# Optimization experiments

Hardware: AMD Instinct MI355X
Metric: run time of the kernel (lower is better)

Reference implementation:

```python
import jax, jax.numpy as jnp
from jax import lax
import numpy as np

CONF_THRES = 0.55
IOU_THRES = 0.45
MAX_DET = 1000
MAX_WH = 7680.0   # class offset for class-aware NMS (agnostic=False)
K = 4096          # NMS candidate cap (yolov5 max_nms analogue, jit-static)
IMG = 640         # letterboxed network input size
B, N, NC = 16, 25200, 80


def setup_inputs() -> dict:
    key = jax.random.key(0)
    k1, k2, k3, k4 = jax.random.split(key, 4)
    cxcy = jax.random.uniform(k1, (B, N, 2), jnp.float32, 0.0, IMG)
    wh = jax.random.uniform(k2, (B, N, 2), jnp.float32, 2.0, 120.0)
    obj = jax.random.uniform(k3, (B, N, 1), jnp.float32) ** 4
    cls = jax.random.uniform(k4, (B, N, NC), jnp.float32)
    pred = jnp.concatenate([cxcy, wh, obj, cls], axis=-1)  # [B, N, 5+NC]
    return {"pred": pred, "img0_h": 1080, "img0_w": 1920}


def xywh2xyxy(x):
    cx, cy, w, h = x[..., 0], x[..., 1], x[..., 2], x[..., 3]
    return jnp.stack([cx - w / 2, cy - h / 2, cx + w / 2, cy + h / 2], axis=-1)


def box_iou(a, b):
    # a: [K,4], b: [K,4] xyxy -> [K,K]
    lt = jnp.maximum(a[:, None, :2], b[None, :, :2])
    rb = jnp.minimum(a[:, None, 2:], b[None, :, 2:])
    wh = jnp.clip(rb - lt, 0.0)
    inter = wh[..., 0] * wh[..., 1]
    area_a = (a[:, 2] - a[:, 0]) * (a[:, 3] - a[:, 1])
    area_b = (b[:, 2] - b[:, 0]) * (b[:, 3] - b[:, 1])
    return inter / (area_a[:, None] + area_b[None, :] - inter + 1e-7)


def _nms_image(p, img0_h, img0_w):
    # p: [N, 5+NC]
    obj = p[:, 4]
    cls_conf = p[:, 5:] * obj[:, None]          # conf = obj * cls
    conf = cls_conf.max(axis=-1)
    cls_id = cls_conf.argmax(axis=-1)
    valid = (obj > CONF_THRES) & (conf > CONF_THRES)
    score = jnp.where(valid, conf, -1.0)
    # top-K candidates, sorted by confidence (descending)
    top_scores, top_idx = lax.top_k(score, K)
    boxes = xywh2xyxy(p[top_idx, :4])           # [K,4]
    cl = cls_id[top_idx].astype(p.dtype)        # [K]
    iou = box_iou(boxes + cl[:, None] * MAX_WH, boxes + cl[:, None] * MAX_WH)
    idx = jnp.arange(K)
    keep0 = top_scores > 0.0

    def body(i, keep):
        # suppress i if a higher-scoring kept box overlaps it too much
        sup = jnp.any(keep & (idx < i) & (iou[:, i] > IOU_THRES))
        return keep.at[i].set(keep[i] & ~sup)

    keep = lax.fori_loop(0, K, body, keep0)
    kept_score = jnp.where(keep, top_scores, -1.0)
    fs, fi = lax.top_k(kept_score, MAX_DET)
    fb = boxes[fi]                              # [MAX_DET,4]
    fc = cl[fi]
    fvalid = fs > 0.0
    # scale_boxes: letterboxed 640x640 -> original img0
    gain = min(IMG / img0_h, IMG / img0_w)
    pad_x = (IMG - img0_w * gain) / 2
    pad_y = (IMG - img0_h * gain) / 2
    fb = (fb - jnp.array([pad_x, pad_y, pad_x, pad_y], fb.dtype)) / gain
    fb = jnp.clip(fb, 0.0, jnp.array([img0_w, img0_h, img0_w, img0_h], fb.dtype))
    fb = jnp.round(fb)
    det = jnp.concatenate([fb, fs[:, None], fc[:, None]], axis=-1)  # [MAX_DET,6]
    return jnp.where(fvalid[:, None], det, 0.0)


def reference(pred, img0_h, img0_w):
    return jax.vmap(lambda p: _nms_image(p, img0_h, img0_w))(pred)
```

## Files before the change

### kernel.cpp

```cpp
#include <hip/hip_runtime.h>

#define BB 16
#define NN 25200
#define NC 80
#define ROWL 85
#define KTOP 4096
#define MAXDET 1000
#define CONF_T 0.55f
#define IOU_T 0.45f
#define MAX_WH_F 7680.0f
#define CNT_STRIDE 32
#define PCNT_STRIDE 16
#define CCAP 256
#define NBIN 2048

#define OFF_CNT   81920
#define OFF_KCNT  83968
#define OFF_BUCK  86016
#define OFF_KEPT  2707456
#define ZERO_WORDS 21504

__global__ void zero_kernel(unsigned int* __restrict__ w) {
  w[blockIdx.x * 256 + threadIdx.x] = 0u;
}

__global__ __launch_bounds__(256) void score_kernel(const float* __restrict__ pred,
                             unsigned long long* __restrict__ buckets,
                             unsigned int* __restrict__ pcnt,
                             unsigned int* __restrict__ cnt) {
  const int b = blockIdx.y;
  const int lane = threadIdx.x & 63;
  const int a0 = blockIdx.x * 256 + (threadIdx.x & ~63);
  const int a = a0 + lane;
  const int g = lane >> 4;
  const int gl = lane & 15;
  const float* __restrict__ pb = pred + (size_t)b * NN * ROWL;
  float obj = 0.0f;
  if (a < NN) obj = pb[(size_t)a * ROWL + 4];
  unsigned long long mask = __ballot(obj > CONF_T);
  unsigned int nvacc = 0;
  while (mask) {
    int s0 = __ffsll(mask) - 1; mask &= mask - 1;
    int s1 = -1, s2 = -1, s3 = -1;
    if (mask) { s1 = __ffsll(mask) - 1; mask &= mask - 1; }
    if (mask) { s2 = __ffsll(mask) - 1; mask &= mask - 1; }
    if (mask) { s3 = __ffsll(mask) - 1; mask &= mask - 1; }
    const int sg = (g == 0) ? s0 : (g == 1) ? s1 : (g == 2) ? s2 : s3;
    const bool act = (sg >= 0);
    const int srow = act ? sg : s0;
    const int aa = a0 + srow;
    const float objg = __shfl(obj, srow, 64);
    const float* __restrict__ row = pb + (size_t)aa * ROWL;
    float best = -1.0f; int bi = gl;
    #pragma unroll
    for (int t = 0; t < 5; ++t) {
      float v = row[5 + gl + 16 * t] * objg;
      if (v > best) { best = v; bi = gl + 16 * t; }
    }
    #pragma unroll
    for (int off = 1; off <= 8; off <<= 1) {
      float ov = __shfl_xor(best, off, 64);
      int oi = __shfl_xor(bi, off, 64);
      if (ov > best || (ov == best && oi < bi)) { best = ov; bi = oi; }
    }
    bool emit = act && (gl == 0) && (best > CONF_T);
    if (emit) {
      unsigned long long key =
          ((unsigned long long)__float_as_uint(best) << 32) |
          ((unsigned long long)((~(unsigned)aa) & 0xFFFFu) << 16) |
          (unsigned long long)(unsigned)bi;
      unsigned int slot = atomicAdd(&pcnt[(b * NC + bi) * PCNT_STRIDE], 1u);
      if (slot < CCAP)
        buckets[((size_t)(b * NC + bi) << 8) + slot] = key;
    }
    unsigned long long em = __ballot(emit);
    if (lane == 0) nvacc += (unsigned int)__popcll(em);
  }
  if (lane == 0 && nvacc)
    atomicAdd(&cnt[b * CNT_STRIDE], nvacc);
}

__device__ __forceinline__ bool iou_sup(float ax1, float ay1, float ax2, float ay2,
                                        float aar, float bx1, float by1, float bx2,
                                        float by2, float bar) {
  float ltx = fmaxf(ax1, bx1), lty = fmaxf(ay1, by1);
  float rbx = fminf(ax2, bx2), rby = fminf(ay2, by2);
  float wv = rbx - ltx; wv = wv > 0.0f ? wv : 0.0f;
  float hv = rby - lty; hv = hv > 0.0f ? hv : 0.0f;
  float inter = wv * hv;
  float iou = inter / (aar + bar - inter + 1e-7f);
  return iou > IOU_T;
}

__global__ __launch_bounds__(64) void class_nms_kernel(
    const float* __restrict__ pred,
    const unsigned long long* __restrict__ buckets,
    const unsigned int* __restrict__ pcnt,
    const unsigned int* __restrict__ cnt,
    unsigned long long* __restrict__ kept,
    unsigned int* __restrict__ kcnt) {
  const int c = blockIdx.x;
  const int b = blockIdx.y;
  const int lane = threadIdx.x;
  unsigned int pc = pcnt[(b * NC + c) * PCNT_STRIDE];
  int n_c = (int)(pc < (unsigned)CCAP ? pc : (unsigned)CCAP);
  const unsigned long long* __restrict__ bk = buckets + ((size_t)(b * NC + c) << 8);
  const float* __restrict__ pb = pred + (size_t)b * NN * ROWL;
  const float offc = (float)c * MAX_WH_F;
  const int count = (int)cnt[b * CNT_STRIDE];

  if (n_c == 0) return;

  if (n_c <= 64 && count <= KTOP) {
    unsigned long long v0 = (lane < n_c) ? bk[lane] : 0ull;
    for (int k2 = 2; k2 <= 64; k2 <<= 1) {
      for (int j = k2 >> 1; j >= 1; j >>= 1) {
        unsigned long long vo = __shfl_xor(v0, j, 64);
        bool desc = ((lane & k2) == 0);
        bool low = ((lane & j) == 0);
        if ((desc == low) ? (vo > v0) : (vo < v0)) v0 = vo;
      }
    }
    float x1 = 0.f, y1 = 0.f, x2 = 0.f, y2 = 0.f, aar = 0.f;
    const bool inr = (lane < n_c);
    if (inr) {
      unsigned int lo = (unsigned int)v0;
      int aa = (int)((~(lo >> 16)) & 0xFFFFu);
      const float* row = pb + (size_t)aa * ROWL;
      float cx = row[0], cy = row[1], w2 = row[2], h2 = row[3];
      x1 = (cx - w2 / 2.0f) + offc;
      y1 = (cy - h2 / 2.0f) + offc;
      x2 = (cx + w2 / 2.0f) + offc;
      y2 = (cy + h2 / 2.0f) + offc;
      aar = (x2 - x1) * (y2 - y1);
    }
    unsigned long long rowreg = 0ull;
    for (int i2 = 0; i2 < n_c; ++i2) {
      float bx1 = __shfl(x1, i2, 64), by1 = __shfl(y1, i2, 64);
      float bx2 = __shfl(x2, i2, 64), by2 = __shfl(y2, i2, 64);
      float bar = __shfl(aar, i2, 64);
      bool sup = inr && (lane > i2) &&
                 iou_sup(bx1, by1, bx2, by2, bar, x1, y1, x2, y2, aar);
      unsigned long long rm = __ballot(sup);
      if (lane == i2) rowreg = rm;
    }
    unsigned long long cand = (n_c >= 64) ? ~0ull : ((1ull << n_c) - 1ull);
    unsigned long long keepm = 0ull;
    while (cand) {
      int i = __ffsll(cand) - 1;
      keepm |= (1ull << i);
      unsigned long long rowi = __shfl(rowreg, i, 64);
      cand &= ~rowi;
      cand &= ~(1ull << i);
    }
    int keep0 = (int)((keepm >> lane) & 1ull);
    unsigned long long m0 = __ballot(keep0 != 0);
    int tot = (int)__popcll(m0);
    unsigned int base3 = 0;
    if (lane == 0) base3 = atomicAdd(&kcnt[b * CNT_STRIDE], (unsigned int)tot);
    base3 = (unsigned int)__shfl((int)base3, 0, 64);
    if (keep0) {
      unsigned int slot = base3 + (unsigned int)__popcll(m0 & ((1ull << lane) - 1ull));
      if (slot < (unsigned)KTOP) kept[(size_t)b * KTOP + slot] = v0;
    }
    return;
  }

  unsigned long long v[4];
  #pragma unroll
  for (int r = 0; r < 4; ++r) {
    int e = (r << 6) + lane;
    v[r] = (e < n_c) ? bk[e] : 0ull;
  }
  if (count > KTOP) {
    unsigned long long T = 0ull;
    for (int bit = 63; bit >= 0; --bit) {
      unsigned long long T2 = T | (1ull << bit);
      int cge = 0;
      for (int c2 = 0; c2 < NC; ++c2) {
        unsigned int p2 = pcnt[(b * NC + c2) * PCNT_STRIDE];
        int n2 = (int)(p2 < (unsigned)CCAP ? p2 : (unsigned)CCAP);
        const unsigned long long* bk2 = buckets + ((size_t)(b * NC + c2) << 8);
        for (int base2 = 0; base2 < n2; base2 += 64) {
          int i = base2 + lane;
          bool ge = (i < n2) && (bk2[i] >= T2);
          cge += (int)__popcll(__ballot(ge));
        }
      }
      if (cge >= KTOP) T = T2;
    }
    #pragma unroll
    for (int r = 0; r < 4; ++r) if (v[r] < T) v[r] = 0ull;
    n_c = 0;
    #pragma unroll
    for (int r = 0; r < 4; ++r) n_c += (int)__popcll(__ballot(v[r] != 0ull));
    if (n_c == 0) return;
  }
  for (int k2 = 2; k2 <= 256; k2 <<= 1) {
    if (k2 == 256) {
      #pragma unroll
      for (int r = 0; r < 2; ++r) {
        unsigned e = (unsigned)((r << 6) + lane);
        bool desc = ((e & k2) == 0);
        unsigned long long lo_ = v[r], hi_ = v[r + 2];
        bool sw = desc ? (lo_ < hi_) : (lo_ > hi_);
        v[r] = sw ? hi_ : lo_; v[r + 2] = sw ? lo_ : hi_;
      }
    }
    if (k2 >= 128) {
      #pragma unroll
      for (int rr = 0; rr < 2; ++rr) {
        int r = rr * 2;
        unsigned e = (unsigned)((r << 6) + lane);
        bool desc = ((e & k2) == 0);
        unsigned long long lo_ = v[r], hi_ = v[r + 1];
        bool sw = desc ? (lo_ < hi_) : (lo_ > hi_);
        v[r] = sw ? hi_ : lo_; v[r + 1] = sw ? lo_ : hi_;
      }
    }
    int j0 = (k2 >> 1) < 32 ? (k2 >> 1) : 32;
    for (int j = j0; j >= 1; j >>= 1) {
      #pragma unroll
      for (int r = 0; r < 4; ++r) {
        unsigned e = (unsigned)((r << 6) + lane);
        unsigned long long vo = __shfl_xor(v[r], j, 64);
        bool desc = ((e & k2) == 0);
        bool low = ((e & j) == 0);
        if ((desc == low) ? (vo > v[r]) : (vo < v[r])) v[r] = vo;
      }
    }
  }
  float x1r[4], y1r[4], x2r[4], y2r[4], ar[4];
  int keepr[4];
  #pragma unroll
  for (int r = 0; r < 4; ++r) {
    int e = (r << 6) + lane;
    keepr[r] = 0; x1r[r] = 0.f; y1r[r] = 0.f; x2r[r] = 0.f; y2r[r] = 0.f; ar[r] = 0.f;
    if (e < n_c) {
      unsigned int lo = (unsigned int)v[r];
      int aa = (int)((~(lo >> 16)) & 0xFFFFu);
      const float* row = pb + (size_t)aa * ROWL;
      float cx = row[0], cy = row[1], w2 = row[2], h2 = row[3];
      x1r[r] = (cx - w2 / 2.0f) + offc;
      y1r[r] = (cy - h2 / 2.0f) + offc;
      x2r[r] = (cx + w2 / 2.0f) + offc;
      y2r[r] = (cy + h2 / 2.0f) + offc;
      ar[r] = (x2r[r] - x1r[r]) * (y2r[r] - y1r[r]);
      keepr[r] = 1;
    }
  }
  for (int i2 = 0; i2 < n_c; ++i2) {
    int ci = i2 >> 6, li = i2 & 63;
    int ki; float bx1v, by1v, bx2v, by2v, bav;
    #define BCAST(R) { ki = __shfl(keepr[R], li, 64); bx1v = __shfl(x1r[R], li, 64); \
                       by1v = __shfl(y1r[R], li, 64); bx2v = __shfl(x2r[R], li, 64); \
                       by2v = __shfl(y2r[R], li, 64); bav = __shfl(ar[R], li, 64); }
    switch (ci) {
      case 0: BCAST(0); break;
      case 1: BCAST(1); break;
      case 2: BCAST(2); break;
      default: BCAST(3); break;
    }
    #undef BCAST
    if (!ki) continue;
    #pragma unroll
    for (int r = 0; r < 4; ++r) {
      int e = (r << 6) + lane;
      if (keepr[r] && e > i2 &&
          iou_sup(bx1v, by1v, bx2v, by2v, bav, x1r[r], y1r[r], x2r[r], y2r[r], ar[r]))
        keepr[r] = 0;
    }
  }
  unsigned long long m[4];
  int tot = 0;
  #pragma unroll
  for (int r = 0; r < 4; ++r) {
    m[r] = __ballot(keepr[r] != 0);
    tot += (int)__popcll(m[r]);
  }
  unsigned int base3 = 0;
  if (lane == 0) base3 = atomicAdd(&kcnt[b * CNT_STRIDE], (unsigned int)tot);
  base3 = (unsigned int)__shfl((int)base3, 0, 64);
  unsigned int start = base3;
  #pragma unroll
  for (int r = 0; r < 4; ++r) {
    if (keepr[r]) {
      unsigned int slot = start + (unsigned int)__popcll(m[r] & ((1ull << lane) - 1ull));
      if (slot < (unsigned)KTOP) kept[(size_t)b * KTOP + slot] = v[r];
    }
    start += (unsigned int)__popcll(m[r]);
  }
}

__global__ __launch_bounds__(1024) void finalize_kernel(
    const float* __restrict__ pred,
    const unsigned long long* __restrict__ kept,
    const unsigned int* __restrict__ kcnt,
    const int* __restrict__ ihp, const int* __restrict__ iwp,
    float* __restrict__ out) {
  __shared__ unsigned int hist[NBIN];
  __shared__ unsigned int sufx[NBIN];
  __shared__ unsigned int curs[NBIN];
  __shared__ unsigned int scanbuf[1024];
  __shared__ unsigned long long skey[KTOP];
  const int b = blockIdx.x;
  const int tid = threadIdx.x;
  unsigned int kcr = kcnt[b * CNT_STRIDE];
  const int kc = (int)(kcr < (unsigned)KTOP ? kcr : (unsigned)KTOP);
  const unsigned long long* __restrict__ kb = kept + (size_t)b * KTOP;

  for (int i = tid; i < NBIN; i += 1024) hist[i] = 0u;
  __syncthreads();

  unsigned long long myk[4];
  int myb[4];
  #pragma unroll
  for (int r = 0; r < 4; ++r) {
    int i = tid + (r << 10);
    myb[r] = -1; myk[r] = 0ull;
    if (i < kc) {
      unsigned long long k = kb[i];
      int bin = (int)((k >> 44) & (unsigned long long)(NBIN - 1));
      myk[r] = k; myb[r] = bin;
      atomicAdd(&hist[bin], 1u);
    }
  }
  __syncthreads();

  unsigned int h0 = hist[2 * tid], h1 = hist[2 * tid + 1];
  unsigned int val = h0 + h1;
  scanbuf[tid] = val;
  __syncthreads();
  for (int off = 1; off < 1024; off <<= 1) {
    unsigned int add = (tid + off < 1024) ? scanbuf[tid + off] : 0u;
    __syncthreads();
    val += add;
    scanbuf[tid] = val;
    __syncthreads();
  }
  unsigned int excl = val - (h0 + h1);
  sufx[2 * tid] = excl + h1;
  sufx[2 * tid + 1] = excl;
  curs[2 * tid] = excl + h1;
  curs[2 * tid + 1] = excl;
  __syncthreads();

  #pragma unroll
  for (int r = 0; r < 4; ++r) {
    if (myb[r] >= 0) {
      unsigned int p = atomicAdd(&curs[myb[r]], 1u);
      skey[p] = myk[r];
    }
  }
  __syncthreads();

  const int h = ihp[0], w3 = iwp[0];
  const double gd = fmin(640.0 / (double)h, 640.0 / (double)w3);
  const float gain = (float)gd;
  const float padx = (float)((640.0 - (double)w3 * gd) * 0.5);
  const float pady = (float)((640.0 - (double)h * gd) * 0.5);
  const float wf = (float)w3, hf = (float)h;
  #pragma unroll
  for (int r = 0; r < 4; ++r) {
    if (myb[r] >= 0) {
      unsigned long long k = myk[r];
      unsigned int gstart = sufx[myb[r]];
      unsigned int gcnt = hist[myb[r]];
      unsigned int rank = gstart;
      for (unsigned int j = 0; j < gcnt; ++j)
        rank += (skey[gstart + j] > k) ? 1u : 0u;
      if (rank < MAXDET) {
        unsigned int lo = (unsigned int)k;
        int aa = (int)((~(lo >> 16)) & 0xFFFFu);
        int cls = (int)(lo & 0xFFFFu);
        float score = __uint_as_float((unsigned int)(k >> 32));
        const float* row = pred + ((size_t)b * NN + aa) * ROWL;
        float cx = row[0], cy = row[1], wd = row[2], ht = row[3];
        float x1 = cx - wd / 2.0f, y1 = cy - ht / 2.0f;
        float x2 = cx + wd / 2.0f, y2 = cy + ht / 2.0f;
        x1 = rintf(fminf(fmaxf((x1 - padx) / gain, 0.0f), wf));
        y1 = rintf(fminf(fmaxf((y1 - pady) / gain, 0.0f), hf));
        x2 = rintf(fminf(fmaxf((x2 - padx) / gain, 0.0f), wf));
        y2 = rintf(fminf(fmaxf((y2 - pady) / gain, 0.0f), hf));
        float* o = out + ((size_t)b * MAXDET + (int)rank) * 6;
        o[0] = x1; o[1] = y1; o[2] = x2; o[3] = y2;
        o[4] = score; o[5] = (float)cls;
      }
    }
  }
  for (int i = kc + tid; i < MAXDET; i += 1024) {
    float* o = out + ((size_t)b * MAXDET + i) * 6;
    o[0] = 0.0f; o[1] = 0.0f; o[2] = 0.0f; o[3] = 0.0f; o[4] = 0.0f; o[5] = 0.0f;
  }
}

extern "C" void kernel_launch(void* const* d_in, const int* in_sizes, int n_in,
                              void* d_out, int out_size, void* d_ws, size_t ws_size,
                              hipStream_t stream) {
  const float* pred = (const float*)d_in[0];
  const int* ih = (const int*)d_in[1];
  const int* iw = (const int*)d_in[2];
  float* out = (float*)d_out;
  char* ws = (char*)d_ws;

  unsigned int* pcnt = (unsigned int*)ws;
  unsigned int* cnt = (unsigned int*)(ws + OFF_CNT);
  unsigned int* kcnt = (unsigned int*)(ws + OFF_KCNT);
  unsigned long long* buckets = (unsigned long long*)(ws + OFF_BUCK);
  unsigned long long* kept = (unsigned long long*)(ws + OFF_KEPT);

  zero_kernel<<<ZERO_WORDS / 256, 256, 0, stream>>>((unsigned int*)ws);
  dim3 sgrid((NN + 255) / 256, BB);
  score_kernel<<<sgrid, 256, 0, stream>>>(pred, buckets, pcnt, cnt);
  dim3 cgrid(NC, BB);
  class_nms_kernel<<<cgrid, 64, 0, stream>>>(pred, buckets, pcnt, cnt, kept, kcnt);
  finalize_kernel<<<BB, 1024, 0, stream>>>(pred, kept, kcnt, ih, iw, out);
}
```

Baseline: 74.15 us.

## Split finalize across multiple blocks per image and use wave-shuffle scan

```diff
diff --git a/kernel.cpp b/kernel.cpp
--- a/kernel.cpp
+++ b/kernel.cpp
@@ -13,6 +13,7 @@
 #define PCNT_STRIDE 16
 #define CCAP 256
 #define NBIN 2048
+#define FBLK 8
 
 #define OFF_CNT   81920
 #define OFF_KCNT  83968
@@ -301,56 +302,53 @@
   __shared__ unsigned int hist[NBIN];
   __shared__ unsigned int sufx[NBIN];
   __shared__ unsigned int curs[NBIN];
-  __shared__ unsigned int scanbuf[1024];
+  __shared__ unsigned int wsum[16], woff[16];
   __shared__ unsigned long long skey[KTOP];
-  const int b = blockIdx.x;
+  const int q = blockIdx.x;
+  const int b = blockIdx.y;
   const int tid = threadIdx.x;
+  const int lane = tid & 63;
+  const int w = tid >> 6;
   unsigned int kcr = kcnt[b * CNT_STRIDE];
   const int kc = (int)(kcr < (unsigned)KTOP ? kcr : (unsigned)KTOP);
   const unsigned long long* __restrict__ kb = kept + (size_t)b * KTOP;
 
-  for (int i = tid; i < NBIN; i += 1024) hist[i] = 0u;
-  __syncthreads();
-
-  unsigned long long myk[4];
-  int myb[4];
+  hist[2 * tid] = 0u; hist[2 * tid + 1] = 0u;
+  __syncthreads();
+
+  for (int i = tid; i < kc; i += 1024) {
+    unsigned long long k = kb[i];
+    atomicAdd(&hist[(int)((k >> 44) & (unsigned long long)(NBIN - 1))], 1u);
+  }
+  __syncthreads();
+
+  unsigned int h0 = hist[2 * tid], h1 = hist[2 * tid + 1];
+  unsigned int v = h0 + h1;
   #pragma unroll
-  for (int r = 0; r < 4; ++r) {
-    int i = tid + (r << 10);
-    myb[r] = -1; myk[r] = 0ull;
-    if (i < kc) {
-      unsigned long long k = kb[i];
-      int bin = (int)((k >> 44) & (unsigned long long)(NBIN - 1));
-      myk[r] = k; myb[r] = bin;
-      atomicAdd(&hist[bin], 1u);
-    }
-  }
-  __syncthreads();
-
-  unsigned int h0 = hist[2 * tid], h1 = hist[2 * tid + 1];
-  unsigned int val = h0 + h1;
-  scanbuf[tid] = val;
-  __syncthreads();
-  for (int off = 1; off < 1024; off <<= 1) {
-    unsigned int add = (tid + off < 1024) ? scanbuf[tid + off] : 0u;
-    __syncthreads();
-    val += add;
-    scanbuf[tid] = val;
-    __syncthreads();
-  }
-  unsigned int excl = val - (h0 + h1);
+  for (int off = 1; off < 64; off <<= 1) {
+    unsigned int o = __shfl_down(v, off, 64);
+    if (lane + off < 64) v += o;
+  }
+  if (lane == 0) wsum[w] = v;
+  __syncthreads();
+  if (tid < 16) {
+    unsigned int s = 0;
+    for (int j = tid + 1; j < 16; ++j) s += wsum[j];
+    woff[tid] = s;
+  }
+  __syncthreads();
+  unsigned int incl = v + woff[w];
+  unsigned int excl = incl - (h0 + h1);
   sufx[2 * tid] = excl + h1;
   sufx[2 * tid + 1] = excl;
   curs[2 * tid] = excl + h1;
   curs[2 * tid + 1] = excl;
   __syncthreads();
 
-  #pragma unroll
-  for (int r = 0; r < 4; ++r) {
-    if (myb[r] >= 0) {
-      unsigned int p = atomicAdd(&curs[myb[r]], 1u);
-      skey[p] = myk[r];
-    }
+  for (int i = tid; i < kc; i += 1024) {
+    unsigned long long k = kb[i];
+    unsigned int p = atomicAdd(&curs[(int)((k >> 44) & (unsigned long long)(NBIN - 1))], 1u);
+    skey[p] = k;
   }
   __syncthreads();
 
@@ -360,37 +358,40 @@
   const float padx = (float)((640.0 - (double)w3 * gd) * 0.5);
   const float pady = (float)((640.0 - (double)h * gd) * 0.5);
   const float wf = (float)w3, hf = (float)h;
-  #pragma unroll
-  for (int r = 0; r < 4; ++r) {
-    if (myb[r] >= 0) {
-      unsigned long long k = myk[r];
-      unsigned int gstart = sufx[myb[r]];
-      unsigned int gcnt = hist[myb[r]];
-      unsigned int rank = gstart;
-      for (unsigned int j = 0; j < gcnt; ++j)
-        rank += (skey[gstart + j] > k) ? 1u : 0u;
-      if (rank < MAXDET) {
-        unsigned int lo = (unsigned int)k;
-        int aa = (int)((~(lo >> 16)) & 0xFFFFu);
-        int cls = (int)(lo & 0xFFFFu);
-        float score = __uint_as_float((unsigned int)(k >> 32));
-        const float* row = pred + ((size_t)b * NN + aa) * ROWL;
-        float cx = row[0], cy = row[1], wd = row[2], ht = row[3];
-        float x1 = cx - wd / 2.0f, y1 = cy - ht / 2.0f;
-        float x2 = cx + wd / 2.0f, y2 = cy + ht / 2.0f;
-        x1 = rintf(fminf(fmaxf((x1 - padx) / gain, 0.0f), wf));
-        y1 = rintf(fminf(fmaxf((y1 - pady) / gain, 0.0f), hf));
-        x2 = rintf(fminf(fmaxf((x2 - padx) / gain, 0.0f), wf));
-        y2 = rintf(fminf(fmaxf((y2 - pady) / gain, 0.0f), hf));
-        float* o = out + ((size_t)b * MAXDET + (int)rank) * 6;
-        o[0] = x1; o[1] = y1; o[2] = x2; o[3] = y2;
-        o[4] = score; o[5] = (float)cls;
-      }
-    }
-  }
-  for (int i = kc + tid; i < MAXDET; i += 1024) {
-    float* o = out + ((size_t)b * MAXDET + i) * 6;
-    o[0] = 0.0f; o[1] = 0.0f; o[2] = 0.0f; o[3] = 0.0f; o[4] = 0.0f; o[5] = 0.0f;
+  const int qlen = (kc + FBLK - 1) / FBLK;
+  const int i = q * qlen + tid;
+  if (tid < qlen && i < kc) {
+    unsigned long long k = kb[i];
+    int bin = (int)((k >> 44) & (unsigned long long)(NBIN - 1));
+    unsigned int gstart = sufx[bin];
+    unsigned int gcnt = hist[bin];
+    unsigned int rank = gstart;
+    for (unsigned int j = 0; j < gcnt; ++j)
+      rank += (skey[gstart + j] > k) ? 1u : 0u;
+    if (rank < MAXDET) {
+      unsigned int lo = (unsigned int)k;
+      int aa = (int)((~(lo >> 16)) & 0xFFFFu);
+      int cls = (int)(lo & 0xFFFFu);
+      float score = __uint_as_float((unsigned int)(k >> 32));
+      const float* row = pred + ((size_t)b * NN + aa) * ROWL;
+      float cx = row[0], cy = row[1], wd = row[2], ht = row[3];
+      float x1 = cx - wd / 2.0f, y1 = cy - ht / 2.0f;
+      float x2 = cx + wd / 2.0f, y2 = cy + ht / 2.0f;
+      x1 = rintf(fminf(fmaxf((x1 - padx) / gain, 0.0f), wf));
+      y1 = rintf(fminf(fmaxf((y1 - pady) / gain, 0.0f), hf));
+      x2 = rintf(fminf(fmaxf((x2 - padx) / gain, 0.0f), wf));
+      y2 = rintf(fminf(fmaxf((y2 - pady) / gain, 0.0f), hf));
+      float* o = out + ((size_t)b * MAXDET + (int)rank) * 6;
+      o[0] = x1; o[1] = y1; o[2] = x2; o[3] = y2;
+      o[4] = score; o[5] = (float)cls;
+    }
+  }
+  {
+    int i2 = kc + q * 1024 + tid;
+    if (i2 < MAXDET) {
+      float* o = out + ((size_t)b * MAXDET + i2) * 6;
+      o[0] = 0.0f; o[1] = 0.0f; o[2] = 0.0f; o[3] = 0.0f; o[4] = 0.0f; o[5] = 0.0f;
+    }
   }
 }
 
@@ -414,5 +415,6 @@
   score_kernel<<<sgrid, 256, 0, stream>>>(pred, buckets, pcnt, cnt);
   dim3 cgrid(NC, BB);
   class_nms_kernel<<<cgrid, 64, 0, stream>>>(pred, buckets, pcnt, cnt, kept, kcnt);
-  finalize_kernel<<<BB, 1024, 0, stream>>>(pred, kept, kcnt, ih, iw, out);
-}
+  dim3 fgrid(FBLK, BB);
+  finalize_kernel<<<fgrid, 1024, 0, stream>>>(pred, kept, kcnt, ih, iw, out);
+}
```

New measurement: 71.17 us (median of 2 runs). -4.0%, faster.
